# Optimization experiments

Measured on AMD Instinct MI355X. Metric: run time of the kernel, lower is better.

## Reference

```python
import jax, jax.numpy as jnp
import numpy as np

B, N, D_IN, D_OUT = 8, 2048, 256, 128
ROW_ZERO = 85 - 10  # hardcoded in original: a[:, 0:85-10] = 0 (zeros rows, dim 1)
NEG_BIG = -9.0e15
EPS = 1e-12  # F.normalize eps


def setup_inputs() -> dict:
    key = jax.random.key(0)
    k1, k2, k3, k4 = jax.random.split(key, 4)
    h = jax.random.normal(k1, (B, N, D_IN), dtype=jnp.float32)
    adj = jax.random.randint(k2, (B, N, N), 0, 2, dtype=jnp.int32)
    adj_eye = jax.random.randint(k3, (B, N, N), 0, 2, dtype=jnp.int32)
    # xavier_uniform with gain=1.414 for W [in, out]
    limit = 1.414 * np.sqrt(6.0 / (D_IN + D_OUT))
    W = jax.random.uniform(k4, (D_IN, D_OUT), minval=-limit, maxval=limit, dtype=jnp.float32)
    return {"h": h, "adj": adj, "adj_eye": adj_eye, "W": W}


def reference(h, adj, adj_eye, W):
    # Wh: [B, N, D_OUT]
    Wh = jnp.matmul(h, W)
    # L2-normalize along feature dim (F.normalize semantics: x / max(||x||, eps))
    norm = jnp.maximum(jnp.linalg.norm(Wh, axis=-1, keepdims=True), EPS)
    Whn = Wh / norm
    # dense cosine-similarity scores: [B, N, N]
    score = jnp.einsum("bnd,bmd->bnm", Whn, Whn)
    # double-sort top-k emulation (faithful to original, incl. row-wise zeroing bug)
    a_sorted = jnp.sort(score, axis=-1)
    idx1 = jnp.argsort(score, axis=-1)
    a_sorted = a_sorted.at[:, 0:ROW_ZERO, :].set(0.0)
    idx2 = jnp.argsort(idx1, axis=-1)  # inverse permutation
    attscore = jnp.take_along_axis(a_sorted, idx2, axis=-1)
    # adjacency mask + softmax over neighbors
    e = jnp.where(adj_eye > 0, attscore, NEG_BIG)
    attention = jax.nn.softmax(e, axis=-1)
    # (dropout is identity in eval mode)
    h_prime = jnp.matmul(attention, Wh)
    return jax.nn.elu(h_prime)
```

## Files before the change

kernel.cpp:

```cpp
#include <hip/hip_runtime.h>
#include <stdint.h>

#define NN   2048
#define DD   128
#define DIN  256
#define ROWZ 75

typedef float f32x4 __attribute__((ext_vector_type(4)));
typedef short bf16x8 __attribute__((ext_vector_type(8)));
typedef unsigned int u32x4 __attribute__((ext_vector_type(4)));
typedef unsigned int u32x2 __attribute__((ext_vector_type(2)));
typedef unsigned long long u64x2 __attribute__((ext_vector_type(2)));

__device__ __forceinline__ unsigned short f2bf(float x){
  union { float f; unsigned int u; } v; v.f = x;
  unsigned int u = v.u;
  u += 0x7fffu + ((u >> 16) & 1u);
  return (unsigned short)(u >> 16);
}
__device__ __forceinline__ float bf2f(unsigned short b){
  union { float f; unsigned int u; } v; v.u = ((unsigned int)b) << 16;
  return v.f;
}

__launch_bounds__(256, 8)
__global__ void pack_kernel(const int* __restrict__ adje,
                            unsigned long long* __restrict__ adjp)
{
  const int t  = threadIdx.x;
  const int wv = t >> 6;
  const int ln = t & 63;
#pragma unroll
  for (int rr = 0; rr < 2; ++rr){
    const int row = blockIdx.x * 8 + wv * 2 + rr;
    const int* arow = adje + (size_t)row * NN;
    unsigned long long* drow = adjp + (size_t)row * 32;
#pragma unroll
    for (int c = 0; c < 4; ++c){
      int pv[8];
#pragma unroll
      for (int j = 0; j < 8; ++j) pv[j] = arow[c*512 + j*64 + ln];
      unsigned long long m[8];
#pragma unroll
      for (int j = 0; j < 8; ++j) m[j] = __ballot(pv[j] > 0);
      if (ln == 0){
#pragma unroll
        for (int j = 0; j < 8; j += 2){
          u64x2 pk = { m[j], m[j+1] };
          *(u64x2*)(drow + c*8 + j) = pk;
        }
      }
    }
  }
}

__launch_bounds__(256, 2)
__global__ void wh_kernel(const float* __restrict__ h, const float* __restrict__ W,
                          unsigned short* __restrict__ whn, unsigned short* __restrict__ whT)
{
  __shared__ float hs[32][36];
  __shared__ float Ws[32][128];
  __shared__ float ssp[32][33];
  __shared__ float sinv[32];

  const int t  = threadIdx.x;
  const int r0 = blockIdx.x * 32;
  const int r4 = (t >> 5) * 4;
  const int d4 = (t & 31) * 4;

  float acc[4][4];
#pragma unroll
  for (int i = 0; i < 4; ++i)
#pragma unroll
    for (int j = 0; j < 4; ++j) acc[i][j] = 0.f;

  const int lrow = t >> 3;
  const int lkb  = (t & 7) * 4;

  for (int kt = 0; kt < 8; ++kt){
    __syncthreads();
    {
      const float* src = h + (size_t)(r0 + lrow) * DIN + kt * 32 + lkb;
      f32x4 a = *(const f32x4*)src;
#pragma unroll
      for (int e = 0; e < 4; ++e) hs[lkb + e][lrow] = a[e];
    }
    {
      const int k = t >> 3;
      const int d = (t & 7) * 16;
      const float* src = W + (size_t)(kt * 32 + k) * DD + d;
      float* dst = &Ws[k][d];
#pragma unroll
      for (int e = 0; e < 4; ++e) ((f32x4*)dst)[e] = ((const f32x4*)src)[e];
    }
    __syncthreads();
#pragma unroll
    for (int k = 0; k < 32; ++k){
      f32x4 w4 = *(const f32x4*)&Ws[k][d4];
      f32x4 ha = *(const f32x4*)&hs[k][r4];
#pragma unroll
      for (int i = 0; i < 4; ++i)
#pragma unroll
        for (int j = 0; j < 4; ++j)
          acc[i][j] += ha[i] * w4[j];
    }
  }

#pragma unroll
  for (int i = 0; i < 4; ++i){
    float s = acc[i][0]*acc[i][0] + acc[i][1]*acc[i][1]
            + acc[i][2]*acc[i][2] + acc[i][3]*acc[i][3];
    ssp[r4 + i][t & 31] = s;
  }
  __syncthreads();
  if (t < 32){
    float ss = 0.f;
#pragma unroll
    for (int c = 0; c < 32; ++c) ss += ssp[t][c];
    sinv[t] = 1.0f / fmaxf(sqrtf(ss), 1e-12f);
  }
  __syncthreads();

  const int bb = r0 >> 11;
  const int n0 = (r0 & 2047) + r4;

#pragma unroll
  for (int i = 0; i < 4; ++i){
    const float inv = sinv[r4 + i];
    unsigned int lo = (unsigned int)f2bf(acc[i][0]*inv) | ((unsigned int)f2bf(acc[i][1]*inv) << 16);
    unsigned int hi = (unsigned int)f2bf(acc[i][2]*inv) | ((unsigned int)f2bf(acc[i][3]*inv) << 16);
    u32x2 pk = { lo, hi };
    *(u32x2*)(whn + (size_t)(r0 + r4 + i) * DD + d4) = pk;
  }
#pragma unroll
  for (int j = 0; j < 4; ++j){
    u32x2 pk;
#pragma unroll
    for (int e = 0; e < 2; ++e)
      pk[e] = (unsigned int)f2bf(acc[2*e][j]) | ((unsigned int)f2bf(acc[2*e + 1][j]) << 16);
    *(u32x2*)(whT + ((size_t)(bb * DD + d4 + j)) * NN + n0) = pk;
  }
}

__launch_bounds__(256, 2)
__global__ void attn_kernel(const unsigned short* __restrict__ whn,
                            const unsigned short* __restrict__ whT,
                            const unsigned int* __restrict__ adjp,
                            float* __restrict__ out)
{
  __shared__ unsigned short Vt[128 * 128];
  __shared__ unsigned short Pbuf[4][32 * 40];
  __shared__ float linv_s[32];
  __shared__ unsigned int Ab[32 * 68];

  const int t    = threadIdx.x;
  const int w    = t >> 6;
  const int l    = t & 63;
  const int quad = l >> 4;
  const int l16  = l & 15;
  const int b     = blockIdx.x & 7;
  const int qbase = (blockIdx.x >> 3) * 32;

  const unsigned short* whn_b = whn + (size_t)b * NN * DD;
  const unsigned short* whT_b = whT + (size_t)b * DD * NN;

  {
    const unsigned int* src = adjp + ((size_t)(b * NN + qbase + (t >> 3))) * 64 + (t & 7) * 8;
    u32x4 a0 = *(const u32x4*)src;
    u32x4 a1 = *(const u32x4*)(src + 4);
    unsigned int* dst = &Ab[(t >> 3) * 68 + (t & 7) * 8];
    *(u32x4*)dst = a0;
    *(u32x4*)(dst + 4) = a1;
  }

  bf16x8 qf[2][4];
#pragma unroll
  for (int s = 0; s < 2; ++s)
#pragma unroll
    for (int kc = 0; kc < 4; ++kc)
      qf[s][kc] = *(const bf16x8*)(whn_b + (size_t)(qbase + s*16 + l16) * DD + kc*32 + quad*8);

  f32x4 oacc[2][8];
  float lacc[2][4];
#pragma unroll
  for (int s = 0; s < 2; ++s){
#pragma unroll
    for (int dt = 0; dt < 8; ++dt) oacc[s][dt] = (f32x4){0.f, 0.f, 0.f, 0.f};
#pragma unroll
    for (int r = 0; r < 4; ++r) lacc[s][r] = 0.f;
  }

  unsigned short* const Pw = &Pbuf[w][0];

  for (int it = 0; it < 16; ++it){
    const int m0 = it * 128;
    __syncthreads();

    bf16x8 kf[2][4];
#pragma unroll
    for (int f = 0; f < 2; ++f)
#pragma unroll
      for (int kc = 0; kc < 4; ++kc)
        kf[f][kc] = *(const bf16x8*)(whn_b + (size_t)(m0 + w*32 + f*16 + l16) * DD + kc*32 + quad*8);

#pragma unroll
    for (int ii = 0; ii < 8; ++ii){
      const int d   = w*32 + ii*4 + quad;
      const int gsw = l16 ^ (d & 7);
      const unsigned short* src = whT_b + (size_t)d * NN + m0 + gsw * 8;
      __builtin_amdgcn_global_load_lds(
          (const __attribute__((address_space(1))) void*)src,
          (__attribute__((address_space(3))) void*)&Vt[(w*32 + ii*4) * 128],
          16, 0, 0);
    }

    unsigned int aw[2][4];
#pragma unroll
    for (int s = 0; s < 2; ++s)
#pragma unroll
      for (int r = 0; r < 4; ++r)
        aw[s][r] = Ab[(s*16 + quad*4 + r) * 68 + it*4 + w];

#pragma unroll
    for (int f = 0; f < 2; ++f){
#pragma unroll
      for (int s = 0; s < 2; ++s){
        f32x4 sc = (f32x4){0.f, 0.f, 0.f, 0.f};
#pragma unroll
        for (int kc = 0; kc < 4; ++kc)
          sc = __builtin_amdgcn_mfma_f32_16x16x32_bf16(qf[s][kc], kf[f][kc], sc, 0, 0, 0);
#pragma unroll
        for (int r = 0; r < 4; ++r){
          const int qrow = qbase + s*16 + quad*4 + r;
          float sv = (qrow < ROWZ) ? 0.f : sc[r];
          float p32 = ((aw[s][r] >> (f*16 + l16)) & 1u) ? __expf(sv) : 0.f;
          unsigned short pb = f2bf(p32);
          lacc[s][r] += bf2f(pb);
          Pw[(s*16 + quad*4 + r) * 40 + f*16 + l16] = pb;
        }
      }
    }
    __syncthreads();

#pragma unroll
    for (int s = 0; s < 2; ++s){
      bf16x8 pfr = *(const bf16x8*)&Pw[(s*16 + l16) * 40 + quad*8];
#pragma unroll
      for (int dt = 0; dt < 8; ++dt){
        const int d  = dt*16 + l16;
        const int gg = (w*4 + quad) ^ (d & 7);
        bf16x8 vf = *(const bf16x8*)&Vt[d * 128 + gg * 8];
        oacc[s][dt] = __builtin_amdgcn_mfma_f32_16x16x32_bf16(pfr, vf, oacc[s][dt], 0, 0, 0);
      }
    }
  }

  {
    float* lredw = (float*)Pw;
#pragma unroll
    for (int s = 0; s < 2; ++s)
#pragma unroll
      for (int r = 0; r < 4; ++r)
        lredw[(s*16 + quad*4 + r) * 16 + l16] = lacc[s][r];
  }
  __syncthreads();
  if (t < 32){
    float sum = 0.f;
    for (int ww = 0; ww < 4; ++ww){
      const float* lr = (const float*)&Pbuf[ww][0];
#pragma unroll
      for (int c = 0; c < 16; ++c) sum += lr[t * 16 + c];
    }
    linv_s[t] = 1.0f / sum;
  }

  float* const ored = (float*)&Vt[0];
  for (int s = 0; s < 2; ++s){
    __syncthreads();
#pragma unroll
    for (int dt = 0; dt < 8; ++dt)
#pragma unroll
      for (int r = 0; r < 4; ++r)
        ored[w*2048 + (quad*4 + r)*128 + dt*16 + l16] = oacc[s][dt][r];
    __syncthreads();
#pragma unroll
    for (int j = 0; j < 8; ++j){
      const int o  = j*256 + t;
      const int ql = o >> 7, d = o & 127;
      float v = ored[ql*128 + d] + ored[2048 + ql*128 + d]
              + ored[4096 + ql*128 + d] + ored[6144 + ql*128 + d];
      v *= linv_s[s*16 + ql];
      v = (v > 0.f) ? v : expm1f(v);
      out[(size_t)(b*NN + qbase + s*16 + ql) * DD + d] = v;
    }
  }
}

extern "C" void kernel_launch(void* const* d_in, const int* in_sizes, int n_in,
                              void* d_out, int out_size, void* d_ws, size_t ws_size,
                              hipStream_t stream)
{
  const float* h       = (const float*)d_in[0];
  const int*   adj_eye = (const int*)d_in[2];
  const float* W       = (const float*)d_in[3];
  float*       out     = (float*)d_out;

  unsigned short* whn  = (unsigned short*)d_ws;
  unsigned short* whT  = whn + (size_t)16384 * 128;
  unsigned int*   adjp = (unsigned int*)(whT + (size_t)16384 * 128);

  pack_kernel<<<2048, 256, 0, stream>>>(adj_eye, (unsigned long long*)adjp);
  wh_kernel<<<512, 256, 0, stream>>>(h, W, whn, whT);
  attn_kernel<<<512, 256, 0, stream>>>(whn, whT, adjp, out);
}
```

Baseline: 322.0 us.

## Double-buffer V tiles and prefetch adjacency and projection operands

The attention kernel now holds two V tile buffers in shared memory. It issues the asynchronous global-to-LDS load for the next 128-key tile while the current tile's scores are computed, and it reads adjacency bit words straight from global memory one iteration ahead instead of staging the whole row block in LDS. The P·V loop shares each V fragment across both query sub-tiles, uses raw s_barrier with sched_barrier fences, and raises wave priority around the MFMAs. The projection kernel also prefetches the next h/W chunk into registers before the compute loop. The cost is doubled V LDS footprint and more live registers, plus a risk that raw barriers do not wait for outstanding LDS DMA.

```diff
diff --git a/kernel.cpp b/kernel.cpp
--- a/kernel.cpp
+++ b/kernel.cpp
@@ -76,24 +76,35 @@
 
   const int lrow = t >> 3;
   const int lkb  = (t & 7) * 4;
+  const int wk   = t >> 3;
+  const int wd   = (t & 7) * 16;
+
+  f32x4 ph = *(const f32x4*)(h + (size_t)(r0 + lrow) * DIN + lkb);
+  f32x4 pW[4];
+  {
+    const float* ws = W + (size_t)wk * DD + wd;
+#pragma unroll
+    for (int e = 0; e < 4; ++e) pW[e] = ((const f32x4*)ws)[e];
+  }
 
   for (int kt = 0; kt < 8; ++kt){
     __syncthreads();
+#pragma unroll
+    for (int e = 0; e < 4; ++e) hs[lkb + e][lrow] = ph[e];
     {
-      const float* src = h + (size_t)(r0 + lrow) * DIN + kt * 32 + lkb;
-      f32x4 a = *(const f32x4*)src;
-#pragma unroll
-      for (int e = 0; e < 4; ++e) hs[lkb + e][lrow] = a[e];
-    }
-    {
-      const int k = t >> 3;
-      const int d = (t & 7) * 16;
-      const float* src = W + (size_t)(kt * 32 + k) * DD + d;
-      float* dst = &Ws[k][d];
-#pragma unroll
-      for (int e = 0; e < 4; ++e) ((f32x4*)dst)[e] = ((const f32x4*)src)[e];
+      f32x4* dst = (f32x4*)&Ws[wk][wd];
+#pragma unroll
+      for (int e = 0; e < 4; ++e) dst[e] = pW[e];
     }
     __syncthreads();
+
+    if (kt < 7){
+      ph = *(const f32x4*)(h + (size_t)(r0 + lrow) * DIN + (kt+1)*32 + lkb);
+      const float* ws = W + (size_t)((kt+1)*32 + wk) * DD + wd;
+#pragma unroll
+      for (int e = 0; e < 4; ++e) pW[e] = ((const f32x4*)ws)[e];
+    }
+
 #pragma unroll
     for (int k = 0; k < 32; ++k){
       f32x4 w4 = *(const f32x4*)&Ws[k][d4];
@@ -148,10 +159,9 @@
                             const unsigned int* __restrict__ adjp,
                             float* __restrict__ out)
 {
-  __shared__ unsigned short Vt[128 * 128];
+  __shared__ unsigned short Vt[2][128 * 128];
   __shared__ unsigned short Pbuf[4][32 * 40];
   __shared__ float linv_s[32];
-  __shared__ unsigned int Ab[32 * 68];
 
   const int t    = threadIdx.x;
   const int w    = t >> 6;
@@ -163,15 +173,7 @@
 
   const unsigned short* whn_b = whn + (size_t)b * NN * DD;
   const unsigned short* whT_b = whT + (size_t)b * DD * NN;
-
-  {
-    const unsigned int* src = adjp + ((size_t)(b * NN + qbase + (t >> 3))) * 64 + (t & 7) * 8;
-    u32x4 a0 = *(const u32x4*)src;
-    u32x4 a1 = *(const u32x4*)(src + 4);
-    unsigned int* dst = &Ab[(t >> 3) * 68 + (t & 7) * 8];
-    *(u32x4*)dst = a0;
-    *(u32x4*)(dst + 4) = a1;
-  }
+  const unsigned int*   adjw  = adjp + ((size_t)(b * NN + qbase)) * 64;
 
   bf16x8 qf[2][4];
 #pragma unroll
@@ -192,9 +194,26 @@
 
   unsigned short* const Pw = &Pbuf[w][0];
 
+#pragma unroll
+  for (int ii = 0; ii < 8; ++ii){
+    const int d   = w*32 + ii*4 + quad;
+    const int gsw = l16 ^ (d & 7);
+    const unsigned short* src = whT_b + (size_t)d * NN + gsw * 8;
+    __builtin_amdgcn_global_load_lds(
+        (const __attribute__((address_space(1))) void*)src,
+        (__attribute__((address_space(3))) void*)&Vt[0][(w*32 + ii*4) * 128],
+        16, 0, 0);
+  }
+  unsigned int aw[2][4];
+#pragma unroll
+  for (int s = 0; s < 2; ++s)
+#pragma unroll
+    for (int r = 0; r < 4; ++r)
+      aw[s][r] = adjw[(size_t)(s*16 + quad*4 + r) * 64 + w];
+
   for (int it = 0; it < 16; ++it){
-    const int m0 = it * 128;
-    __syncthreads();
+    const int m0  = it * 128;
+    const int cur = it & 1;
 
     bf16x8 kf[2][4];
 #pragma unroll
@@ -203,23 +222,24 @@
       for (int kc = 0; kc < 4; ++kc)
         kf[f][kc] = *(const bf16x8*)(whn_b + (size_t)(m0 + w*32 + f*16 + l16) * DD + kc*32 + quad*8);
 
-#pragma unroll
-    for (int ii = 0; ii < 8; ++ii){
-      const int d   = w*32 + ii*4 + quad;
-      const int gsw = l16 ^ (d & 7);
-      const unsigned short* src = whT_b + (size_t)d * NN + m0 + gsw * 8;
-      __builtin_amdgcn_global_load_lds(
-          (const __attribute__((address_space(1))) void*)src,
-          (__attribute__((address_space(3))) void*)&Vt[(w*32 + ii*4) * 128],
-          16, 0, 0);
-    }
-
-    unsigned int aw[2][4];
-#pragma unroll
-    for (int s = 0; s < 2; ++s)
-#pragma unroll
-      for (int r = 0; r < 4; ++r)
-        aw[s][r] = Ab[(s*16 + quad*4 + r) * 68 + it*4 + w];
+    unsigned int awn[2][4];
+    if (it < 15){
+#pragma unroll
+      for (int s = 0; s < 2; ++s)
+#pragma unroll
+        for (int r = 0; r < 4; ++r)
+          awn[s][r] = adjw[(size_t)(s*16 + quad*4 + r) * 64 + (it+1)*4 + w];
+#pragma unroll
+      for (int ii = 0; ii < 8; ++ii){
+        const int d   = w*32 + ii*4 + quad;
+        const int gsw = l16 ^ (d & 7);
+        const unsigned short* src = whT_b + (size_t)d * NN + (m0 + 128) + gsw * 8;
+        __builtin_amdgcn_global_load_lds(
+            (const __attribute__((address_space(1))) void*)src,
+            (__attribute__((address_space(3))) void*)&Vt[cur ^ 1][(w*32 + ii*4) * 128],
+            16, 0, 0);
+      }
+    }
 
 #pragma unroll
     for (int f = 0; f < 2; ++f){
@@ -240,18 +260,34 @@
         }
       }
     }
-    __syncthreads();
-
-#pragma unroll
-    for (int s = 0; s < 2; ++s){
-      bf16x8 pfr = *(const bf16x8*)&Pw[(s*16 + l16) * 40 + quad*8];
-#pragma unroll
-      for (int dt = 0; dt < 8; ++dt){
-        const int d  = dt*16 + l16;
-        const int gg = (w*4 + quad) ^ (d & 7);
-        bf16x8 vf = *(const bf16x8*)&Vt[d * 128 + gg * 8];
-        oacc[s][dt] = __builtin_amdgcn_mfma_f32_16x16x32_bf16(pfr, vf, oacc[s][dt], 0, 0, 0);
-      }
+
+    __builtin_amdgcn_sched_barrier(0);
+    __builtin_amdgcn_s_barrier();
+    __builtin_amdgcn_sched_barrier(0);
+
+    bf16x8 pfr0 = *(const bf16x8*)&Pw[(l16) * 40 + quad*8];
+    bf16x8 pfr1 = *(const bf16x8*)&Pw[(16 + l16) * 40 + quad*8];
+    __builtin_amdgcn_s_setprio(1);
+#pragma unroll
+    for (int dt = 0; dt < 8; ++dt){
+      const int d  = dt*16 + l16;
+      const int gg = (w*4 + quad) ^ (d & 7);
+      bf16x8 vf = *(const bf16x8*)&Vt[cur][d * 128 + gg * 8];
+      oacc[0][dt] = __builtin_amdgcn_mfma_f32_16x16x32_bf16(pfr0, vf, oacc[0][dt], 0, 0, 0);
+      oacc[1][dt] = __builtin_amdgcn_mfma_f32_16x16x32_bf16(pfr1, vf, oacc[1][dt], 0, 0, 0);
+    }
+    __builtin_amdgcn_s_setprio(0);
+
+    __builtin_amdgcn_sched_barrier(0);
+    __builtin_amdgcn_s_barrier();
+    __builtin_amdgcn_sched_barrier(0);
+
+    if (it < 15){
+#pragma unroll
+      for (int s = 0; s < 2; ++s)
+#pragma unroll
+        for (int r = 0; r < 4; ++r)
+          aw[s][r] = awn[s][r];
     }
   }
 
@@ -274,7 +310,7 @@
     linv_s[t] = 1.0f / sum;
   }
 
-  float* const ored = (float*)&Vt[0];
+  float* const ored = (float*)&Vt[0][0];
   for (int s = 0; s < 2; ++s){
     __syncthreads();
 #pragma unroll
```

After: 329.8 us. 2.4% more time.
